# Kernel optimization log

Hardware: AMD Instinct MI355X
Metric: run time of the kernel (lower is better)

Reference implementation:

```python
import jax, jax.numpy as jnp
import numpy as np

EPS = 0.3  # residual scaling from init_kwargs
N, E = 50000, 800000
IN_DIM, HID, OUT = 256, 64, 40


def setup_inputs() -> dict:
    key = jax.random.key(0)
    ks = jax.random.split(key, 8)
    h = jax.random.normal(ks[0], (N, IN_DIM), dtype=jnp.float32)
    src = jax.random.randint(ks[1], (E,), 0, N, dtype=jnp.int32)
    dst = jax.random.randint(ks[2], (E,), 0, N, dtype=jnp.int32)
    t1_w = jax.random.normal(ks[3], (HID, IN_DIM), dtype=jnp.float32) * 0.05
    t1_b = jnp.zeros((HID,), jnp.float32)
    gate_w1 = jax.random.normal(ks[4], (2 * HID,), dtype=jnp.float32) * 0.1
    gate_b1 = jnp.zeros((1,), jnp.float32)
    gate_w2 = jax.random.normal(ks[5], (2 * HID,), dtype=jnp.float32) * 0.1
    gate_b2 = jnp.zeros((1,), jnp.float32)
    t2_w = jax.random.normal(ks[6], (OUT, HID), dtype=jnp.float32) * 0.05
    t2_b = jnp.zeros((OUT,), jnp.float32)
    return {"h": h, "src": src, "dst": dst, "t1_w": t1_w, "t1_b": t1_b,
            "gate_w1": gate_w1, "gate_b1": gate_b1,
            "gate_w2": gate_w2, "gate_b2": gate_b2,
            "t2_w": t2_w, "t2_b": t2_b}


def _fa_layer(x, src, dst, d, gate_w, gate_b):
    # gate over concat([h_dst, h_src]) == h_dst @ w[:H] + h_src @ w[H:]
    H = x.shape[1]
    g = jnp.tanh(x[dst] @ gate_w[:H] + x[src] @ gate_w[H:] + gate_b[0])  # [E]
    e = g * d[dst] * d[src]                                              # [E]
    # message: u_mul_e('h','e') then sum onto dst
    z = jnp.zeros_like(x).at[dst].add(x[src] * e[:, None])               # [N,H]
    return z


def reference(h, src, dst, t1_w, t1_b, gate_w1, gate_b1, gate_w2, gate_b2, t2_w, t2_b):
    n = h.shape[0]
    # degree normalization d = deg^{-1/2} (in-degree, clamped to >=1)
    deg = jnp.zeros((n,), h.dtype).at[dst].add(jnp.ones_like(dst, h.dtype))
    d = jax.lax.rsqrt(jnp.maximum(deg, 1.0))
    # dropout is identity in eval mode
    x = jax.nn.relu(h @ t1_w.T + t1_b)
    raw = x
    for gw, gb in ((gate_w1, gate_b1), (gate_w2, gate_b2)):
        x = EPS * raw + _fa_layer(x, src, dst, d, gw, gb)
    logits = x @ t2_w.T + t2_b
    return jax.nn.log_softmax(logits, axis=1)
```

## Files before the change

kernel.cpp:

```cpp
#include <hip/hip_runtime.h>
#include <hip/hip_bf16.h>
#include <math.h>

#define IN_DIM 256
#define HID 64
#define OUT_DIM 40
#define EPS_RES 0.3f
#define NBUK 256
#define CAP 5120
#define EPB 2048

typedef __attribute__((ext_vector_type(8))) short short8v;
typedef __attribute__((ext_vector_type(4))) float f32x4;

__device__ __forceinline__ float tanh_fast(float u) {
    float t = __expf(2.0f * u);
    return 1.0f - 2.0f / (t + 1.0f);
}

__device__ __forceinline__ short f2bf(float f) {
    __hip_bfloat16 b = __float2bfloat16(f);
    return __builtin_bit_cast(short, b);
}

__device__ __forceinline__ float bf2f(unsigned short u) {
    return __builtin_bit_cast(float, (unsigned int)u << 16);
}

__global__ void k_wconv(const float* __restrict__ w1, const float* __restrict__ w2,
                        short* __restrict__ wpre, short* __restrict__ w2p,
                        int* __restrict__ bcur) {
    int i = blockIdx.x * blockDim.x + threadIdx.x;
    if (i < HID * IN_DIM) wpre[i] = f2bf(w1[i]);
    if (i < 48 * HID) {
        int row = i >> 6;
        w2p[i] = f2bf(row < OUT_DIM ? w2[i] : 0.f);
    }
    if (i < NBUK) bcur[i] = 0;
}

__global__ __launch_bounds__(256) void k_bscatter(
    const int* __restrict__ src, const int* __restrict__ dst,
    int* __restrict__ bcur, unsigned int* __restrict__ edges, int E) {
    __shared__ int cnt[NBUK];
    __shared__ int lcur[NBUK];
    int tid = threadIdx.x;
    cnt[tid] = 0;
    __syncthreads();
    int base = blockIdx.x * EPB;
#pragma unroll 8
    for (int k = 0; k < EPB / 256; ++k) {
        int i = base + k * 256 + tid;
        if (i < E) atomicAdd(&cnt[dst[i] >> 8], 1);
    }
    __syncthreads();
    if (cnt[tid]) lcur[tid] = tid * CAP + atomicAdd(&bcur[tid], cnt[tid]);
    __syncthreads();
#pragma unroll 8
    for (int k = 0; k < EPB / 256; ++k) {
        int i = base + k * 256 + tid;
        if (i < E) {
            int d = dst[i];
            int p = atomicAdd(&lcur[d >> 8], 1);
            edges[p] = ((unsigned int)(d & 255) << 16) | (unsigned int)src[i];
        }
    }
}

__global__ __launch_bounds__(256) void k_bfine(
    unsigned int* __restrict__ edges, const int* __restrict__ bcur,
    int* __restrict__ rowp, int* __restrict__ rowe,
    float* __restrict__ dinv, int N) {
    __shared__ unsigned int buf[CAP];
    __shared__ int lc[NBUK];
    __shared__ int sm[NBUK];
    __shared__ int lcur[NBUK];
    int tid = threadIdx.x;
    int b = blockIdx.x;
    int start = b * CAP;
    int cnt = bcur[b];
    lc[tid] = 0;
    __syncthreads();
    for (int k = tid; k < cnt; k += 256) {
        unsigned int v = edges[start + k];
        buf[k] = v;
        atomicAdd(&lc[(v >> 16) & 255], 1);
    }
    __syncthreads();
    int v = lc[tid];
    sm[tid] = v;
    __syncthreads();
    for (int off = 1; off < NBUK; off <<= 1) {
        int t = (tid >= off) ? sm[tid - off] : 0;
        __syncthreads();
        sm[tid] += t;
        __syncthreads();
    }
    int ls = sm[tid] - v;
    lcur[tid] = ls;
    int node = b * 256 + tid;
    if (node < N) {
        rowp[node] = start + ls;
        rowe[node] = start + ls + v;
        dinv[node] = rsqrtf(fmaxf((float)v, 1.0f));
    }
    __syncthreads();
    for (int k = tid; k < cnt; k += 256) {
        unsigned int pv = buf[k];
        int lo = (pv >> 16) & 255;
        int p = atomicAdd(&lcur[lo], 1);
        edges[start + p] = pv & 0xFFFFu;
    }
}

__global__ __launch_bounds__(256) void k_gemm1(
    const float* __restrict__ h, const short* __restrict__ wpre,
    const float* __restrict__ b, const float* __restrict__ gw,
    const float* __restrict__ dinv,
    float* __restrict__ out, short* __restrict__ xsb0,
    float* __restrict__ gpa, float* __restrict__ gpb, int N) {
    int tid = threadIdx.x;
    int lane = tid & 63;
    int l15 = lane & 15, lhi = lane >> 4;
    int wv = __builtin_amdgcn_readfirstlane(tid >> 6);
    int base = blockIdx.x * 64 + wv * 16;

    int ra = base + l15;
    if (ra >= N) ra = N - 1;
    const float* arow = h + (size_t)ra * IN_DIM + lhi * 8;

    f32x4 acc[4] = {{0.f,0.f,0.f,0.f},{0.f,0.f,0.f,0.f},
                    {0.f,0.f,0.f,0.f},{0.f,0.f,0.f,0.f}};

#pragma unroll
    for (int ks = 0; ks < 8; ++ks) {
        const float4* ap = (const float4*)(arow + ks * 32);
        float4 a0 = ap[0], a1 = ap[1];
        short8v af;
        af[0] = f2bf(a0.x); af[1] = f2bf(a0.y);
        af[2] = f2bf(a0.z); af[3] = f2bf(a0.w);
        af[4] = f2bf(a1.x); af[5] = f2bf(a1.y);
        af[6] = f2bf(a1.z); af[7] = f2bf(a1.w);

        const short* wk = wpre + (size_t)l15 * IN_DIM + ks * 32 + lhi * 8;
#pragma unroll
        for (int t = 0; t < 4; ++t) {
            short8v bf = *(const short8v*)(wk + t * 16 * IN_DIM);
            acc[t] = __builtin_amdgcn_mfma_f32_16x16x32_bf16(af, bf, acc[t], 0, 0, 0);
        }
    }

#pragma unroll
    for (int r = 0; r < 4; ++r) {
        int grow = base + lhi * 4 + r;
        float vals[4];
        float pa = 0.f, pb = 0.f;
#pragma unroll
        for (int t = 0; t < 4; ++t) {
            int col = t * 16 + l15;
            float v = fmaxf(acc[t][r] + b[col], 0.f);
            vals[t] = v;
            pa = fmaf(v, gw[col], pa);
            pb = fmaf(v, gw[HID + col], pb);
        }
        if (grow < N) {
            float dv = dinv[grow];
            float* o  = out + (size_t)grow * HID;
            short* os = xsb0 + (size_t)grow * HID;
#pragma unroll
            for (int t = 0; t < 4; ++t) {
                o[t * 16 + l15]  = vals[t];
                os[t * 16 + l15] = f2bf(vals[t] * dv);
            }
        }
#pragma unroll
        for (int m = 1; m < 16; m <<= 1) {
            pa += __shfl_xor(pa, m);
            pb += __shfl_xor(pb, m);
        }
        if (l15 == 0 && grow < N) {
            gpa[grow] = pa;
            gpb[grow] = pb;
        }
    }
}

__global__ __launch_bounds__(256) void k_gather(
    const int* __restrict__ rowp, const int* __restrict__ rowe,
    const int* __restrict__ ssrc,
    const float* __restrict__ gpa, const float* __restrict__ gpb,
    const float* __restrict__ dinv, const float* __restrict__ gbias,
    const unsigned short* __restrict__ xsb, const float* __restrict__ raw,
    short* __restrict__ zb, int scaled,
    const float* __restrict__ gw_next, float* __restrict__ gpa_next,
    float* __restrict__ gpb_next, int N) {
    int lane = threadIdx.x & 63;
    int wv = __builtin_amdgcn_readfirstlane(threadIdx.x >> 6);
    int t = blockIdx.x * 4 + wv;
    if (t >= N) return;

    float at = gpa[t] + gbias[0];
    float dt = dinv[t];
    float acc = EPS_RES * raw[((size_t)t << 6) + lane];
    float acc2 = 0.f;
    int k0 = rowp[t];
    int end = rowe[t];

    for (int kc = k0; kc < end; kc += 64) {
        int cnt = end - kc;
        if (cnt > 64) cnt = 64;
        int idx = kc + ((lane < cnt) ? lane : 0);
        int sv = ssrc[idx];
        float ev = tanh_fast(at + gpb[sv]) * dt;
        int evi = __builtin_bit_cast(int, ev);
        int j = 0;
        for (; j + 4 <= cnt; j += 4) {
            int s0 = __builtin_amdgcn_readlane(sv, j);
            int s1 = __builtin_amdgcn_readlane(sv, j + 1);
            int s2 = __builtin_amdgcn_readlane(sv, j + 2);
            int s3 = __builtin_amdgcn_readlane(sv, j + 3);
            float e0 = __builtin_bit_cast(float, __builtin_amdgcn_readlane(evi, j));
            float e1 = __builtin_bit_cast(float, __builtin_amdgcn_readlane(evi, j + 1));
            float e2 = __builtin_bit_cast(float, __builtin_amdgcn_readlane(evi, j + 2));
            float e3 = __builtin_bit_cast(float, __builtin_amdgcn_readlane(evi, j + 3));
            float x0 = bf2f(xsb[((size_t)s0 << 6) + lane]);
            float x1 = bf2f(xsb[((size_t)s1 << 6) + lane]);
            float x2 = bf2f(xsb[((size_t)s2 << 6) + lane]);
            float x3 = bf2f(xsb[((size_t)s3 << 6) + lane]);
            acc  = fmaf(e0, x0, acc);
            acc2 = fmaf(e1, x1, acc2);
            acc  = fmaf(e2, x2, acc);
            acc2 = fmaf(e3, x3, acc2);
        }
        for (; j < cnt; ++j) {
            int s0 = __builtin_amdgcn_readlane(sv, j);
            float e0 = __builtin_bit_cast(float, __builtin_amdgcn_readlane(evi, j));
            acc = fmaf(e0, bf2f(xsb[((size_t)s0 << 6) + lane]), acc);
        }
    }
    acc += acc2;
    zb[((size_t)t << 6) + lane] = f2bf(scaled ? dt * acc : acc);

    if (gw_next) {
        float pa = acc * gw_next[lane];
        float pb = acc * gw_next[HID + lane];
#pragma unroll
        for (int m = 32; m; m >>= 1) {
            pa += __shfl_xor(pa, m);
            pb += __shfl_xor(pb, m);
        }
        if (lane == 0) {
            gpa_next[t] = pa;
            gpb_next[t] = pb;
        }
    }
}

__global__ __launch_bounds__(256) void k_head(
    const unsigned short* __restrict__ xb, const short* __restrict__ w2p,
    const float* __restrict__ b2, float* __restrict__ out, int N) {
    int tid = threadIdx.x;
    int lane = tid & 63;
    int l15 = lane & 15, lhi = lane >> 4;
    int wv = __builtin_amdgcn_readfirstlane(tid >> 6);
    int base = blockIdx.x * 64 + wv * 16;

    int ra = base + l15;
    if (ra >= N) ra = N - 1;
    const short* arow = (const short*)(xb + (size_t)ra * HID + lhi * 8);

    f32x4 acc[3] = {{0.f,0.f,0.f,0.f},{0.f,0.f,0.f,0.f},{0.f,0.f,0.f,0.f}};

#pragma unroll
    for (int ks = 0; ks < 2; ++ks) {
        short8v af = *(const short8v*)(arow + ks * 32);
        const short* wk = w2p + (size_t)l15 * HID + ks * 32 + lhi * 8;
#pragma unroll
        for (int t = 0; t < 3; ++t) {
            short8v bf = *(const short8v*)(wk + t * 16 * HID);
            acc[t] = __builtin_amdgcn_mfma_f32_16x16x32_bf16(af, bf, acc[t], 0, 0, 0);
        }
    }

    bool has2 = (l15 < 8);
    float b0 = b2[l15];
    float b1 = b2[l15 + 16];
    float bq = has2 ? b2[l15 + 32] : 0.f;

#pragma unroll
    for (int r = 0; r < 4; ++r) {
        int grow = base + lhi * 4 + r;
        float v0 = acc[0][r] + b0;
        float v1 = acc[1][r] + b1;
        float v2 = acc[2][r] + bq;
        float m = fmaxf(fmaxf(v0, v1), has2 ? v2 : -1e30f);
#pragma unroll
        for (int mm = 1; mm < 16; mm <<= 1) m = fmaxf(m, __shfl_xor(m, mm));
        float s = expf(v0 - m) + expf(v1 - m) + (has2 ? expf(v2 - m) : 0.f);
#pragma unroll
        for (int mm = 1; mm < 16; mm <<= 1) s += __shfl_xor(s, mm);
        float lse = m + logf(s);
        if (grow < N) {
            float* o = out + (size_t)grow * OUT_DIM;
            o[l15] = v0 - lse;
            o[l15 + 16] = v1 - lse;
            if (has2) o[l15 + 32] = v2 - lse;
        }
    }
}

extern "C" void kernel_launch(void* const* d_in, const int* in_sizes, int n_in,
                              void* d_out, int out_size, void* d_ws, size_t ws_size,
                              hipStream_t stream) {
    const float* h    = (const float*)d_in[0];
    const int*   src  = (const int*)d_in[1];
    const int*   dst  = (const int*)d_in[2];
    const float* t1_w = (const float*)d_in[3];
    const float* t1_b = (const float*)d_in[4];
    const float* gw1  = (const float*)d_in[5];
    const float* gb1  = (const float*)d_in[6];
    const float* gw2  = (const float*)d_in[7];
    const float* gb2  = (const float*)d_in[8];
    const float* t2_w = (const float*)d_in[9];
    const float* t2_b = (const float*)d_in[10];
    float* out = (float*)d_out;

    const int N = in_sizes[0] / IN_DIM;
    const int E = in_sizes[1];
    const int NEB = (E + EPB - 1) / EPB;
    const int NBB = (N + 255) / 256;

    float* ws   = (float*)d_ws;
    float* raw  = ws;
    short* xsb0 = (short*)(raw + (size_t)N * HID);
    short* xsb1 = xsb0 + (size_t)N * HID;
    short* xBb  = xsb0;
    float* dinv = (float*)(xsb1 + (size_t)N * HID);
    float* gpa1 = dinv + N;
    float* gpb1 = gpa1 + N;
    float* gpa2 = gpb1 + N;
    float* gpb2 = gpa2 + N;
    short* wpre = (short*)(gpb2 + N);
    short* w2p  = wpre + HID * IN_DIM;
    int* rowp   = (int*)(w2p + 48 * HID);
    int* rowe   = rowp + N;
    int* bcur   = rowe + N;
    unsigned int* edges = (unsigned int*)(bcur + NBUK);

    const int TB = 256;

    k_wconv<<<(HID * IN_DIM + TB - 1) / TB, TB, 0, stream>>>(t1_w, t2_w, wpre, w2p, bcur);

    k_bscatter<<<NEB, TB, 0, stream>>>(src, dst, bcur, edges, E);
    k_bfine<<<NBB, TB, 0, stream>>>(edges, bcur, rowp, rowe, dinv, N);

    k_gemm1<<<(N + 63) / 64, TB, 0, stream>>>(h, wpre, t1_b, gw1, dinv,
                                              raw, xsb0, gpa1, gpb1, N);

    k_gather<<<(N + 3) / 4, TB, 0, stream>>>(rowp, rowe, (const int*)edges,
                                             gpa1, gpb1, dinv, gb1,
                                             (const unsigned short*)xsb0, raw,
                                             xsb1, 1, gw2, gpa2, gpb2, N);

    k_gather<<<(N + 3) / 4, TB, 0, stream>>>(rowp, rowe, (const int*)edges,
                                             gpa2, gpb2, dinv, gb2,
                                             (const unsigned short*)xsb1, raw,
                                             xBb, 0, nullptr, nullptr, nullptr, N);

    k_head<<<(N + 63) / 64, TB, 0, stream>>>((const unsigned short*)xBb, w2p, t2_b, out, N);
}
```

Before: 133.1 us.

## Store raw residual in bf16, widen gather unroll, vectorize bucket loads, halve EPB

The residual activation raw is now stored as bf16 instead of fp32, which halves its write in gemm1 and its reads in both gather passes. The gather inner loop goes from 4 to 8 outstanding row loads with four independent accumulators, plus a 2-wide tail, to expose more memory-level parallelism. k_bfine loads edges as uint4 vectors, and k_bscatter uses 1024 edges per block for more blocks. The bf16 residual adds rounding error, and the uint4 load assumes 16-byte alignment of each bucket start, which holds since CAP is a multiple of 4.

```diff
diff --git a/kernel.cpp b/kernel.cpp
--- a/kernel.cpp
+++ b/kernel.cpp
@@ -8,7 +8,7 @@
 #define EPS_RES 0.3f
 #define NBUK 256
 #define CAP 5120
-#define EPB 2048
+#define EPB 1024
 
 typedef __attribute__((ext_vector_type(8))) short short8v;
 typedef __attribute__((ext_vector_type(4))) float f32x4;
@@ -48,7 +48,7 @@
     cnt[tid] = 0;
     __syncthreads();
     int base = blockIdx.x * EPB;
-#pragma unroll 8
+#pragma unroll 4
     for (int k = 0; k < EPB / 256; ++k) {
         int i = base + k * 256 + tid;
         if (i < E) atomicAdd(&cnt[dst[i] >> 8], 1);
@@ -56,7 +56,7 @@
     __syncthreads();
     if (cnt[tid]) lcur[tid] = tid * CAP + atomicAdd(&bcur[tid], cnt[tid]);
     __syncthreads();
-#pragma unroll 8
+#pragma unroll 4
     for (int k = 0; k < EPB / 256; ++k) {
         int i = base + k * 256 + tid;
         if (i < E) {
@@ -81,10 +81,17 @@
     int cnt = bcur[b];
     lc[tid] = 0;
     __syncthreads();
-    for (int k = tid; k < cnt; k += 256) {
-        unsigned int v = edges[start + k];
-        buf[k] = v;
-        atomicAdd(&lc[(v >> 16) & 255], 1);
+    for (int k4 = tid * 4; k4 < cnt; k4 += 1024) {
+        uint4 v = *(const uint4*)&edges[start + k4];
+#pragma unroll
+        for (int m = 0; m < 4; ++m) {
+            int k = k4 + m;
+            if (k < cnt) {
+                unsigned int pv = ((const unsigned int*)&v)[m];
+                buf[k] = pv;
+                atomicAdd(&lc[(pv >> 16) & 255], 1);
+            }
+        }
     }
     __syncthreads();
     int v = lc[tid];
@@ -117,7 +124,7 @@
     const float* __restrict__ h, const short* __restrict__ wpre,
     const float* __restrict__ b, const float* __restrict__ gw,
     const float* __restrict__ dinv,
-    float* __restrict__ out, short* __restrict__ xsb0,
+    short* __restrict__ rawb, short* __restrict__ xsb0,
     float* __restrict__ gpa, float* __restrict__ gpb, int N) {
     int tid = threadIdx.x;
     int lane = tid & 63;
@@ -165,11 +172,11 @@
         }
         if (grow < N) {
             float dv = dinv[grow];
-            float* o  = out + (size_t)grow * HID;
+            short* o  = rawb + (size_t)grow * HID;
             short* os = xsb0 + (size_t)grow * HID;
 #pragma unroll
             for (int t = 0; t < 4; ++t) {
-                o[t * 16 + l15]  = vals[t];
+                o[t * 16 + l15]  = f2bf(vals[t]);
                 os[t * 16 + l15] = f2bf(vals[t] * dv);
             }
         }
@@ -190,7 +197,7 @@
     const int* __restrict__ ssrc,
     const float* __restrict__ gpa, const float* __restrict__ gpb,
     const float* __restrict__ dinv, const float* __restrict__ gbias,
-    const unsigned short* __restrict__ xsb, const float* __restrict__ raw,
+    const unsigned short* __restrict__ xsb, const unsigned short* __restrict__ rawb,
     short* __restrict__ zb, int scaled,
     const float* __restrict__ gw_next, float* __restrict__ gpa_next,
     float* __restrict__ gpb_next, int N) {
@@ -201,8 +208,8 @@
 
     float at = gpa[t] + gbias[0];
     float dt = dinv[t];
-    float acc = EPS_RES * raw[((size_t)t << 6) + lane];
-    float acc2 = 0.f;
+    float a0v = EPS_RES * bf2f(rawb[((size_t)t << 6) + lane]);
+    float a1v = 0.f, a2v = 0.f, a3v = 0.f;
     int k0 = rowp[t];
     int end = rowe[t];
 
@@ -214,31 +221,57 @@
         float ev = tanh_fast(at + gpb[sv]) * dt;
         int evi = __builtin_bit_cast(int, ev);
         int j = 0;
-        for (; j + 4 <= cnt; j += 4) {
+        for (; j + 8 <= cnt; j += 8) {
             int s0 = __builtin_amdgcn_readlane(sv, j);
             int s1 = __builtin_amdgcn_readlane(sv, j + 1);
             int s2 = __builtin_amdgcn_readlane(sv, j + 2);
             int s3 = __builtin_amdgcn_readlane(sv, j + 3);
+            int s4 = __builtin_amdgcn_readlane(sv, j + 4);
+            int s5 = __builtin_amdgcn_readlane(sv, j + 5);
+            int s6 = __builtin_amdgcn_readlane(sv, j + 6);
+            int s7 = __builtin_amdgcn_readlane(sv, j + 7);
             float e0 = __builtin_bit_cast(float, __builtin_amdgcn_readlane(evi, j));
             float e1 = __builtin_bit_cast(float, __builtin_amdgcn_readlane(evi, j + 1));
             float e2 = __builtin_bit_cast(float, __builtin_amdgcn_readlane(evi, j + 2));
             float e3 = __builtin_bit_cast(float, __builtin_amdgcn_readlane(evi, j + 3));
+            float e4 = __builtin_bit_cast(float, __builtin_amdgcn_readlane(evi, j + 4));
+            float e5 = __builtin_bit_cast(float, __builtin_amdgcn_readlane(evi, j + 5));
+            float e6 = __builtin_bit_cast(float, __builtin_amdgcn_readlane(evi, j + 6));
+            float e7 = __builtin_bit_cast(float, __builtin_amdgcn_readlane(evi, j + 7));
             float x0 = bf2f(xsb[((size_t)s0 << 6) + lane]);
             float x1 = bf2f(xsb[((size_t)s1 << 6) + lane]);
             float x2 = bf2f(xsb[((size_t)s2 << 6) + lane]);
             float x3 = bf2f(xsb[((size_t)s3 << 6) + lane]);
-            acc  = fmaf(e0, x0, acc);
-            acc2 = fmaf(e1, x1, acc2);
-            acc  = fmaf(e2, x2, acc);
-            acc2 = fmaf(e3, x3, acc2);
-        }
-        for (; j < cnt; ++j) {
+            float x4 = bf2f(xsb[((size_t)s4 << 6) + lane]);
+            float x5 = bf2f(xsb[((size_t)s5 << 6) + lane]);
+            float x6 = bf2f(xsb[((size_t)s6 << 6) + lane]);
+            float x7 = bf2f(xsb[((size_t)s7 << 6) + lane]);
+            a0v = fmaf(e0, x0, a0v);
+            a1v = fmaf(e1, x1, a1v);
+            a2v = fmaf(e2, x2, a2v);
+            a3v = fmaf(e3, x3, a3v);
+            a0v = fmaf(e4, x4, a0v);
+            a1v = fmaf(e5, x5, a1v);
+            a2v = fmaf(e6, x6, a2v);
+            a3v = fmaf(e7, x7, a3v);
+        }
+        for (; j + 2 <= cnt; j += 2) {
+            int s0 = __builtin_amdgcn_readlane(sv, j);
+            int s1 = __builtin_amdgcn_readlane(sv, j + 1);
+            float e0 = __builtin_bit_cast(float, __builtin_amdgcn_readlane(evi, j));
+            float e1 = __builtin_bit_cast(float, __builtin_amdgcn_readlane(evi, j + 1));
+            float x0 = bf2f(xsb[((size_t)s0 << 6) + lane]);
+            float x1 = bf2f(xsb[((size_t)s1 << 6) + lane]);
+            a0v = fmaf(e0, x0, a0v);
+            a1v = fmaf(e1, x1, a1v);
+        }
+        if (j < cnt) {
             int s0 = __builtin_amdgcn_readlane(sv, j);
             float e0 = __builtin_bit_cast(float, __builtin_amdgcn_readlane(evi, j));
-            acc = fmaf(e0, bf2f(xsb[((size_t)s0 << 6) + lane]), acc);
-        }
-    }
-    acc += acc2;
+            a0v = fmaf(e0, bf2f(xsb[((size_t)s0 << 6) + lane]), a0v);
+        }
+    }
+    float acc = (a0v + a1v) + (a2v + a3v);
     zb[((size_t)t << 6) + lane] = f2bf(scaled ? dt * acc : acc);
 
     if (gw_next) {
@@ -330,9 +363,8 @@
     const int NEB = (E + EPB - 1) / EPB;
     const int NBB = (N + 255) / 256;
 
-    float* ws   = (float*)d_ws;
-    float* raw  = ws;
-    short* xsb0 = (short*)(raw + (size_t)N * HID);
+    short* rawb = (short*)d_ws;
+    short* xsb0 = rawb + (size_t)N * HID;
     short* xsb1 = xsb0 + (size_t)N * HID;
     short* xBb  = xsb0;
     float* dinv = (float*)(xsb1 + (size_t)N * HID);
@@ -355,16 +387,18 @@
     k_bfine<<<NBB, TB, 0, stream>>>(edges, bcur, rowp, rowe, dinv, N);
 
     k_gemm1<<<(N + 63) / 64, TB, 0, stream>>>(h, wpre, t1_b, gw1, dinv,
-                                              raw, xsb0, gpa1, gpb1, N);
+                                              rawb, xsb0, gpa1, gpb1, N);
 
     k_gather<<<(N + 3) / 4, TB, 0, stream>>>(rowp, rowe, (const int*)edges,
                                              gpa1, gpb1, dinv, gb1,
-                                             (const unsigned short*)xsb0, raw,
+                                             (const unsigned short*)xsb0,
+                                             (const unsigned short*)rawb,
                                              xsb1, 1, gw2, gpa2, gpb2, N);
 
     k_gather<<<(N + 3) / 4, TB, 0, stream>>>(rowp, rowe, (const int*)edges,
                                              gpa2, gpb2, dinv, gb2,
-                                             (const unsigned short*)xsb1, raw,
+                                             (const unsigned short*)xsb1,
+                                             (const unsigned short*)rawb,
                                              xBb, 0, nullptr, nullptr, nullptr, N);
 
     k_head<<<(N + 63) / 64, TB, 0, stream>>>((const unsigned short*)xBb, w2p, t2_b, out, N);
```

After: 130.2 us. 1.02x faster.
